# Kernel tuning notes

Measured on AMD Instinct MI355X. Metric: run time of the kernel, lower is better.

The kernel has to match this reference:

```python
import jax, jax.numpy as jnp
import numpy as np

B, C, H, W = 8, 128, 128, 128
C5 = 5 * C


def setup_inputs() -> dict:
    key = jax.random.key(0)
    ks = jax.random.split(key, 9)
    s_dw = 0.1   # depthwise weight scale
    s_pw = 0.02  # pointwise weight scale
    return {
        "x": jax.random.normal(ks[0], (B, C, H, W), jnp.float32),
        "w1": jax.random.normal(ks[1], (C5, 1, 1, 1), jnp.float32) * s_dw,
        "b1": jax.random.normal(ks[2], (C5,), jnp.float32) * 0.01,
        "w2": jax.random.normal(ks[3], (C5, 1, 3, 3), jnp.float32) * s_dw,
        "b2": jax.random.normal(ks[4], (C5,), jnp.float32) * 0.01,
        "w3": jax.random.normal(ks[5], (C5, 1, 3, 3), jnp.float32) * s_dw,
        "b3": jax.random.normal(ks[6], (C5,), jnp.float32) * 0.01,
        "w4": jax.random.normal(ks[7], (C, C5, 1, 1), jnp.float32) * s_pw,
        "b4": jax.random.normal(ks[8], (C,), jnp.float32) * 0.01,
    }


def nnstacking(x):
    # pad H,W by 1 then stack the 4-neighborhood + center along channels -> 5C
    p = jnp.pad(x, ((0, 0), (0, 0), (1, 1), (1, 1)))
    return jnp.concatenate(
        [p[:, :, 2:, 1:-1],   # neighbor below (i+1, j)
         p[:, :, :-2, 1:-1],  # neighbor above (i-1, j)
         p[:, :, 1:-1, 2:],   # neighbor right (i, j+1)
         p[:, :, 1:-1, :-2],  # neighbor left  (i, j-1)
         p[:, :, 1:-1, 1:-1]],  # center
        axis=1)


def _conv(x, w, b, dilation, padding, groups):
    y = jax.lax.conv_general_dilated(
        x, w, window_strides=(1, 1),
        padding=[(padding, padding), (padding, padding)],
        rhs_dilation=(dilation, dilation),
        dimension_numbers=("NCHW", "OIHW", "NCHW"),
        feature_group_count=groups)
    return y + b[None, :, None, None]


def reference(x, w1, b1, w2, b2, w3, b3, w4, b4):
    shortcut = x
    s = nnstacking(x)  # (B, 5C, H, W)
    # three depthwise branches (groups = 5C): 1x1 rate-1, 3x3 dil-8, 3x3 dil-12
    y = (_conv(s, w1, b1, 1, 0, C5)
         + _conv(s, w2, b2, 8, 8, C5)
         + _conv(s, w3, b3, 12, 12, C5))
    # pointwise 5C -> C, then residual add
    return _conv(y, w4, b4, 1, 0, 1) + shortcut
```

## Files before the change

### kernel.cpp

```cpp
#include <hip/hip_runtime.h>
#include <stdint.h>
#include <stddef.h>


static constexpr int Cc  = 128;
static constexpr int C5  = 640;
static constexpr int Hh  = 128;
static constexpr int Ww  = 128;
static constexpr int LC  = 160;
static constexpr int GR  = 42;
static constexpr int PSz = GR * LC + 8;

typedef __attribute__((ext_vector_type(8))) short short8;
typedef __attribute__((ext_vector_type(4))) float f32x4;

__device__ __forceinline__ uint16_t f2bf(float f) {
  uint32_t b = __float_as_uint(f);
  b += 0x7fffu + ((b >> 16) & 1u);
  return (uint16_t)(b >> 16);
}
__device__ __forceinline__ float bflo(uint32_t v) { return __uint_as_float(v << 16); }
__device__ __forceinline__ float bfhi(uint32_t v) { return __uint_as_float(v & 0xffff0000u); }

__device__ __forceinline__ void async16(uint16_t* lds, const uint16_t* gm) {
  __builtin_amdgcn_global_load_lds(
      (const __attribute__((address_space(1))) uint32_t*)gm,
      (__attribute__((address_space(3))) uint32_t*)lds, 16, 0, 0);
}

__global__ void prep_kernel(const float* __restrict__ w1, const float* __restrict__ b1,
                            const float* __restrict__ w2, const float* __restrict__ b2,
                            const float* __restrict__ w3, const float* __restrict__ b3,
                            const float* __restrict__ w4,
                            uint16_t* __restrict__ w4b, float* __restrict__ cw2,
                            float* __restrict__ cw3, float* __restrict__ bsum) {
  int i = blockIdx.x * 256 + threadIdx.x;
  if (i < Cc * C5) w4b[i] = f2bf(w4[i]);
  if (i < C5) {
    bsum[i] = b1[i] + b2[i] + b3[i];
#pragma unroll
    for (int t = 0; t < 9; ++t) {
      float a = w2[i * 9 + t];
      if (t == 4) a += w1[i] + w3[i * 9 + 4];
      cw2[i * 9 + t] = a;
      cw3[i * 9 + t] = w3[i * 9 + t];
    }
  }
}

__global__ __launch_bounds__(256, 2) void dw_kernel(
    const float* __restrict__ x, const float* __restrict__ cw2,
    const float* __restrict__ cw3, const float* __restrict__ bsum,
    uint16_t* __restrict__ y, int b0) {
  __shared__ uint16_t xs[4 * PSz];

  const int band = blockIdx.x;
  const int g    = blockIdx.y;
  const int bl   = blockIdx.z;
  const int bb   = b0 + bl;
  const int i0   = band * 16;
  const int tid  = threadIdx.x;

#pragma unroll
  for (int it = 0; it < 27; ++it) {
    int idx = it * 256 + tid;
    if (idx < 6720) {
      int col4 = idx % 40;
      int rr   = (idx / 40) % 42;
      int cel  = idx / 1680;
      int gi = i0 - 13 + rr;
      int gj = col4 * 4 - 16;
      float4 v = make_float4(0.f, 0.f, 0.f, 0.f);
      if ((unsigned)gi < 128u && col4 >= 4 && col4 < 36) {
        v = *(const float4*)(x + (((size_t)(bb * Cc + g * 4 + cel) * Hh + gi) << 7) + gj);
      }
      ushort4 h;
      h.x = f2bf(v.x); h.y = f2bf(v.y); h.z = f2bf(v.z); h.w = f2bf(v.w);
      *(ushort4*)(xs + cel * PSz + rr * LC + col4 * 4) = h;
    }
  }
  __syncthreads();

  const int ce = tid & 3;
  const int jt = (tid >> 2) & 7;
  const int ir = tid >> 5;
  const int j0 = jt * 16;
  const int c  = g * 4 + ce;

  float rb[48];
#define LOAD_RB(ROW)                                                      \
  do {                                                                    \
    const uint16_t* _p = xs + ce * PSz + (ROW) * LC + j0;                 \
    _Pragma("unroll") for (int _u = 0; _u < 6; ++_u) {                    \
      uint4 _q = *(const uint4*)(_p + _u * 8);                            \
      rb[_u * 8 + 0] = bflo(_q.x); rb[_u * 8 + 1] = bfhi(_q.x);           \
      rb[_u * 8 + 2] = bflo(_q.y); rb[_u * 8 + 3] = bfhi(_q.y);           \
      rb[_u * 8 + 4] = bflo(_q.z); rb[_u * 8 + 5] = bfhi(_q.z);           \
      rb[_u * 8 + 6] = bflo(_q.w); rb[_u * 8 + 7] = bfhi(_q.w);           \
    }                                                                     \
  } while (0)

  {
    float w2r[3][9], w3r[3][9], bs[3];
    const int msA[3] = {4, 2, 3};
#pragma unroll
    for (int mi = 0; mi < 3; ++mi) {
      int k = msA[mi] * Cc + c;
#pragma unroll
      for (int t = 0; t < 9; ++t) {
        w2r[mi][t] = cw2[k * 9 + t];
        w3r[mi][t] = cw3[k * 9 + t];
      }
      bs[mi] = bsum[k];
    }

#pragma unroll
    for (int it2 = 0; it2 < 2; ++it2) {
      const int i     = i0 + ir + 8 * it2;
      const int rbase = ir + 8 * it2 + 13;
      float acc[3][16];
#pragma unroll
      for (int mi = 0; mi < 3; ++mi)
#pragma unroll
        for (int jj = 0; jj < 16; ++jj) acc[mi][jj] = bs[mi];

#define AROW3(DLT, WARR, UB, DD)                                          \
      do {                                                                \
        LOAD_RB(rbase + (DLT));                                           \
        _Pragma("unroll") for (int mi = 0; mi < 3; ++mi) {                \
          const int aj = (mi == 0) ? 0 : ((mi == 1) ? 1 : -1);            \
          _Pragma("unroll") for (int v = 0; v < 3; ++v) {                 \
            const float w = WARR[mi][(UB) + v];                           \
            const int e = 16 + (DD) * (v - 1) + aj;                       \
            _Pragma("unroll") for (int jj = 0; jj < 16; ++jj)             \
              acc[mi][jj] += w * rb[e + jj];                              \
          }                                                               \
        }                                                                 \
      } while (0)

      AROW3(-12, w3r, 0, 12);
      if (j0 == 0)   acc[1][11] -= w3r[1][0] * rb[16];
      if (j0 == 112) acc[2][4]  -= w3r[2][2] * rb[31];

      AROW3(-8, w2r, 0, 8);
      if (j0 == 0)   acc[1][7]  -= w2r[1][0] * rb[16];
      if (j0 == 112) acc[2][8]  -= w2r[2][2] * rb[31];

      {
        LOAD_RB(rbase);
#pragma unroll
        for (int mi = 0; mi < 3; ++mi) {
          const int aj = (mi == 0) ? 0 : ((mi == 1) ? 1 : -1);
#pragma unroll
          for (int v = 0; v < 3; ++v) {
            const float w = w2r[mi][3 + v];
            const int e = 16 + 8 * (v - 1) + aj;
#pragma unroll
            for (int jj = 0; jj < 16; ++jj) acc[mi][jj] += w * rb[e + jj];
          }
          {
            const float w = w3r[mi][3]; const int e = 4 + aj;
#pragma unroll
            for (int jj = 0; jj < 16; ++jj) acc[mi][jj] += w * rb[e + jj];
          }
          {
            const float w = w3r[mi][5]; const int e = 28 + aj;
#pragma unroll
            for (int jj = 0; jj < 16; ++jj) acc[mi][jj] += w * rb[e + jj];
          }
        }
        if (j0 == 0)   { acc[1][7] -= w2r[1][3] * rb[16]; acc[1][11] -= w3r[1][3] * rb[16]; }
        if (j0 == 112) { acc[2][8] -= w2r[2][5] * rb[31]; acc[2][4]  -= w3r[2][5] * rb[31]; }
      }

      AROW3(8, w2r, 6, 8);
      if (j0 == 0)   acc[1][7]  -= w2r[1][6] * rb[16];
      if (j0 == 112) acc[2][8]  -= w2r[2][8] * rb[31];

      AROW3(12, w3r, 6, 12);
      if (j0 == 0)   acc[1][11] -= w3r[1][6] * rb[16];
      if (j0 == 112) acc[2][4]  -= w3r[2][8] * rb[31];
#undef AROW3

#pragma unroll
      for (int mi = 0; mi < 3; ++mi) {
        const int msA_[3] = {4, 2, 3};
        int k4 = msA_[mi] * 32 + g;
        size_t base = (((size_t)(bl * 160 + k4) << 14) + (size_t)i * Ww + j0) * 4 + ce;
#pragma unroll
        for (int jj = 0; jj < 16; ++jj) y[base + jj * 4] = f2bf(acc[mi][jj]);
      }
    }
  }

  {
    float w2r[2][9], w3r[2][9], bs[2];
#pragma unroll
    for (int mi = 0; mi < 2; ++mi) {
      int k = mi * Cc + c;
#pragma unroll
      for (int t = 0; t < 9; ++t) {
        w2r[mi][t] = cw2[k * 9 + t];
        w3r[mi][t] = cw3[k * 9 + t];
      }
      bs[mi] = bsum[k];
    }

#pragma unroll
    for (int it2 = 0; it2 < 2; ++it2) {
      const int i     = i0 + ir + 8 * it2;
      const int rbase = ir + 8 * it2 + 13;
      float acc[2][16];
#pragma unroll
      for (int mi = 0; mi < 2; ++mi)
#pragma unroll
        for (int jj = 0; jj < 16; ++jj) acc[mi][jj] = bs[mi];

#define BROW3(MI, DLT, WARR, UB, DD, BADROW)                              \
      do {                                                                \
        LOAD_RB(rbase + (DLT));                                           \
        const float sel = ((i + (DLT)) == (BADROW)) ? 0.f : 1.f;          \
        _Pragma("unroll") for (int v = 0; v < 3; ++v) {                   \
          const float w = WARR[MI][(UB) + v] * sel;                       \
          const int e = 16 + (DD) * (v - 1);                              \
          _Pragma("unroll") for (int jj = 0; jj < 16; ++jj)               \
            acc[MI][jj] += w * rb[e + jj];                                \
        }                                                                 \
      } while (0)

#define BROWC(MI, DLT, BADROW)                                            \
      do {                                                                \
        LOAD_RB(rbase + (DLT));                                           \
        const float sel = ((i + (DLT)) == (BADROW)) ? 0.f : 1.f;          \
        _Pragma("unroll") for (int v = 0; v < 3; ++v) {                   \
          const float w = w2r[MI][3 + v] * sel;                           \
          const int e = 16 + 8 * (v - 1);                                 \
          _Pragma("unroll") for (int jj = 0; jj < 16; ++jj)               \
            acc[MI][jj] += w * rb[e + jj];                                \
        }                                                                 \
        {                                                                 \
          const float w = w3r[MI][3] * sel;                               \
          _Pragma("unroll") for (int jj = 0; jj < 16; ++jj)               \
            acc[MI][jj] += w * rb[4 + jj];                                \
        }                                                                 \
        {                                                                 \
          const float w = w3r[MI][5] * sel;                               \
          _Pragma("unroll") for (int jj = 0; jj < 16; ++jj)               \
            acc[MI][jj] += w * rb[28 + jj];                               \
        }                                                                 \
      } while (0)

      BROW3(0, -11, w3r, 0, 12, 0);
      BROW3(0, -7,  w2r, 0, 8, 0);
      BROWC(0, 1, 0);
      BROW3(0, 9,   w2r, 6, 8, 0);
      BROW3(0, 13,  w3r, 6, 12, 0);
      BROW3(1, -13, w3r, 0, 12, 127);
      BROW3(1, -9,  w2r, 0, 8, 127);
      BROWC(1, -1, 127);
      BROW3(1, 7,   w2r, 6, 8, 127);
      BROW3(1, 11,  w3r, 6, 12, 127);
#undef BROW3
#undef BROWC

#pragma unroll
      for (int mi = 0; mi < 2; ++mi) {
        int k4 = mi * 32 + g;
        size_t base = (((size_t)(bl * 160 + k4) << 14) + (size_t)i * Ww + j0) * 4 + ce;
#pragma unroll
        for (int jj = 0; jj < 16; ++jj) y[base + jj * 4] = f2bf(acc[mi][jj]);
      }
    }
  }
#undef LOAD_RB
}

__global__ __launch_bounds__(256, 2) void gemm_kernel(
    const uint16_t* __restrict__ w4b, const uint16_t* __restrict__ y,
    const float* __restrict__ x, const float* __restrict__ b4,
    float* __restrict__ out, int b0) {
  __shared__ uint16_t As[128 * 64];
  __shared__ uint16_t Bs[16 * 128 * 4];

  const int tid  = threadIdx.x;
  const int lane = tid & 63;
  const int wave = tid >> 6;
  const int p0   = blockIdx.x * 128;
  const int bl   = blockIdx.y;
  const int bb   = b0 + bl;

  const int col = lane & 15;
  const int q   = lane >> 4;
  const int o_base = (wave >> 1) * 64;
  const int p_base = (wave & 1) * 64;

  f32x4 acc[4][4];
#pragma unroll
  for (int fm = 0; fm < 4; ++fm)
#pragma unroll
    for (int fn = 0; fn < 4; ++fn) acc[fm][fn] = (f32x4){0.f, 0.f, 0.f, 0.f};

  for (int kt = 0; kt < 10; ++kt) {
#pragma unroll
    for (int l = 0; l < 4; ++l) {
      int u  = (wave * 4 + l) * 64 + lane;
      int o  = u >> 3, ch = u & 7;
      async16(As + u * 8, w4b + (size_t)o * 640 + kt * 64 + ch * 8);
    }
#pragma unroll
    for (int l = 0; l < 4; ++l) {
      int k4t = wave * 4 + l;
      async16(Bs + (k4t * 64 + lane) * 8,
              y + (((size_t)(bl * 160 + kt * 16 + k4t) << 14) + p0) * 4 + lane * 8);
    }
    __syncthreads();

#pragma unroll
    for (int kk = 0; kk < 2; ++kk) {
      short8 af[4], bf[4];
#pragma unroll
      for (int fm = 0; fm < 4; ++fm) {
        int o = o_base + fm * 16 + col;
        af[fm] = *(const short8*)(As + o * 64 + kk * 32 + q * 8);
      }
#pragma unroll
      for (int fn = 0; fn < 4; ++fn) {
        int p = p_base + fn * 16 + col;
        union { short8 s; uint32_t u[4]; } bu;
        const uint32_t* lo = (const uint32_t*)(Bs + ((kk * 8 + 2 * q) * 128 + p) * 4);
        const uint32_t* hi = (const uint32_t*)(Bs + ((kk * 8 + 2 * q + 1) * 128 + p) * 4);
        bu.u[0] = lo[0]; bu.u[1] = lo[1]; bu.u[2] = hi[0]; bu.u[3] = hi[1];
        bf[fn] = bu.s;
      }
#pragma unroll
      for (int fm = 0; fm < 4; ++fm)
#pragma unroll
        for (int fn = 0; fn < 4; ++fn)
          acc[fm][fn] = __builtin_amdgcn_mfma_f32_16x16x32_bf16(af[fm], bf[fn], acc[fm][fn], 0, 0, 0);
    }
    __syncthreads();
  }

#pragma unroll
  for (int fm = 0; fm < 4; ++fm) {
#pragma unroll
    for (int fn = 0; fn < 4; ++fn) {
      int pg = p0 + p_base + fn * 16 + col;
#pragma unroll
      for (int r = 0; r < 4; ++r) {
        int oo = o_base + fm * 16 + q * 4 + r;
        size_t oi = ((size_t)(bb * 128 + oo) << 14) + pg;
        out[oi] = acc[fm][fn][r] + b4[oo] + x[oi];
      }
    }
  }
}

extern "C" void kernel_launch(void* const* d_in, const int* in_sizes, int n_in,
                              void* d_out, int out_size, void* d_ws, size_t ws_size,
                              hipStream_t stream) {
  const float* x  = (const float*)d_in[0];
  const float* w1 = (const float*)d_in[1];
  const float* b1 = (const float*)d_in[2];
  const float* w2 = (const float*)d_in[3];
  const float* b2 = (const float*)d_in[4];
  const float* w3 = (const float*)d_in[5];
  const float* b3 = (const float*)d_in[6];
  const float* w4 = (const float*)d_in[7];
  const float* b4 = (const float*)d_in[8];
  float* out = (float*)d_out;

  char* ws = (char*)d_ws;
  uint16_t* w4b  = (uint16_t*)ws;
  float*    cw2  = (float*)(ws + 163840);
  float*    cw3  = (float*)(ws + 186880);
  float*    bsum = (float*)(ws + 209920);
  uint16_t* y    = (uint16_t*)(ws + (1 << 20));

  const size_t per_b = (size_t)160 * 16384 * 4 * 2;
  int nbc = 4;
  while (nbc > 1 && (size_t)(1 << 20) + (size_t)nbc * per_b > ws_size) nbc >>= 1;

  hipLaunchKernelGGL(prep_kernel, dim3(320), dim3(256), 0, stream,
                     w1, b1, w2, b2, w3, b3, w4, w4b, cw2, cw3, bsum);
  for (int b0 = 0; b0 < 8; b0 += nbc) {
    int nb = (8 - b0) < nbc ? (8 - b0) : nbc;
    hipLaunchKernelGGL(dw_kernel, dim3(8, 32, nb), dim3(256), 0, stream,
                       x, cw2, cw3, bsum, y, b0);
    hipLaunchKernelGGL(gemm_kernel, dim3(128, nb), dim3(256), 0, stream,
                       w4b, y, x, b4, out, b0);
  }
}
```

Baseline: 334.1 us.

## Load GEMM operands directly from global into registers with double buffering

The pointwise GEMM kernel no longer stages A and B tiles in LDS. Each wave now loads its MFMA fragments straight from global memory into registers, with a two-stage register double buffer that prefetches the next K tile while the current one is multiplied, and all __syncthreads are gone. Launch bounds drop to one block per CU to make room for the extra registers. The batch chunk size is raised to 8 so the depthwise and GEMM kernels each run over all batches in one launch when the workspace allows it. The risks are uncoalesced, redundant global reads (each wave re-reads operands other waves also need), lower occupancy, and a larger workspace footprint.

```diff
diff --git a/kernel.cpp b/kernel.cpp
--- a/kernel.cpp
+++ b/kernel.cpp
@@ -21,12 +21,6 @@
 }
 __device__ __forceinline__ float bflo(uint32_t v) { return __uint_as_float(v << 16); }
 __device__ __forceinline__ float bfhi(uint32_t v) { return __uint_as_float(v & 0xffff0000u); }
-
-__device__ __forceinline__ void async16(uint16_t* lds, const uint16_t* gm) {
-  __builtin_amdgcn_global_load_lds(
-      (const __attribute__((address_space(1))) uint32_t*)gm,
-      (__attribute__((address_space(3))) uint32_t*)lds, 16, 0, 0);
-}
 
 __global__ void prep_kernel(const float* __restrict__ w1, const float* __restrict__ b1,
                             const float* __restrict__ w2, const float* __restrict__ b2,
@@ -275,13 +269,10 @@
 #undef LOAD_RB
 }
 
-__global__ __launch_bounds__(256, 2) void gemm_kernel(
+__global__ __launch_bounds__(256, 1) void gemm_kernel(
     const uint16_t* __restrict__ w4b, const uint16_t* __restrict__ y,
     const float* __restrict__ x, const float* __restrict__ b4,
     float* __restrict__ out, int b0) {
-  __shared__ uint16_t As[128 * 64];
-  __shared__ uint16_t Bs[16 * 128 * 4];
-
   const int tid  = threadIdx.x;
   const int lane = tid & 63;
   const int wave = tid >> 6;
@@ -300,46 +291,60 @@
 #pragma unroll
     for (int fn = 0; fn < 4; ++fn) acc[fm][fn] = (f32x4){0.f, 0.f, 0.f, 0.f};
 
-  for (int kt = 0; kt < 10; ++kt) {
-#pragma unroll
-    for (int l = 0; l < 4; ++l) {
-      int u  = (wave * 4 + l) * 64 + lane;
-      int o  = u >> 3, ch = u & 7;
-      async16(As + u * 8, w4b + (size_t)o * 640 + kt * 64 + ch * 8);
-    }
-#pragma unroll
-    for (int l = 0; l < 4; ++l) {
-      int k4t = wave * 4 + l;
-      async16(Bs + (k4t * 64 + lane) * 8,
-              y + (((size_t)(bl * 160 + kt * 16 + k4t) << 14) + p0) * 4 + lane * 8);
-    }
-    __syncthreads();
-
-#pragma unroll
-    for (int kk = 0; kk < 2; ++kk) {
-      short8 af[4], bf[4];
-#pragma unroll
-      for (int fm = 0; fm < 4; ++fm) {
-        int o = o_base + fm * 16 + col;
-        af[fm] = *(const short8*)(As + o * 64 + kk * 32 + q * 8);
-      }
-#pragma unroll
-      for (int fn = 0; fn < 4; ++fn) {
-        int p = p_base + fn * 16 + col;
-        union { short8 s; uint32_t u[4]; } bu;
-        const uint32_t* lo = (const uint32_t*)(Bs + ((kk * 8 + 2 * q) * 128 + p) * 4);
-        const uint32_t* hi = (const uint32_t*)(Bs + ((kk * 8 + 2 * q + 1) * 128 + p) * 4);
-        bu.u[0] = lo[0]; bu.u[1] = lo[1]; bu.u[2] = hi[0]; bu.u[3] = hi[1];
-        bf[fn] = bu.s;
-      }
-#pragma unroll
-      for (int fm = 0; fm < 4; ++fm)
-#pragma unroll
-        for (int fn = 0; fn < 4; ++fn)
-          acc[fm][fn] = __builtin_amdgcn_mfma_f32_16x16x32_bf16(af[fm], bf[fn], acc[fm][fn], 0, 0, 0);
-    }
-    __syncthreads();
-  }
+#define LOADA(AF, KT, KK)                                                   \
+  do {                                                                      \
+    _Pragma("unroll") for (int fm = 0; fm < 4; ++fm) {                      \
+      int o = o_base + fm * 16 + col;                                       \
+      AF[fm] = *(const short8*)(w4b + (size_t)o * 640 + (KT) * 64 +         \
+                                (KK) * 32 + q * 8);                         \
+    }                                                                       \
+  } while (0)
+
+#define LOADB(BF, KT, KK)                                                   \
+  do {                                                                      \
+    _Pragma("unroll") for (int fn = 0; fn < 4; ++fn) {                      \
+      int p = p0 + p_base + fn * 16 + col;                                  \
+      size_t rlo = (((size_t)(bl * 160 + (KT) * 16 + (KK) * 8 + 2 * q)      \
+                     << 14) + p) * 4;                                       \
+      union { short8 s; uint32_t u[4]; } bu;                                \
+      const uint32_t* lo = (const uint32_t*)(y + rlo);                      \
+      const uint32_t* hi = (const uint32_t*)(y + rlo + ((size_t)1 << 16));  \
+      bu.u[0] = lo[0]; bu.u[1] = lo[1]; bu.u[2] = hi[0]; bu.u[3] = hi[1];   \
+      BF[fn] = bu.s;                                                        \
+    }                                                                       \
+  } while (0)
+
+#define MFMAS(AF0, BF0, AF1, BF1)                                           \
+  do {                                                                      \
+    _Pragma("unroll") for (int fm = 0; fm < 4; ++fm)                        \
+      _Pragma("unroll") for (int fn = 0; fn < 4; ++fn)                      \
+        acc[fm][fn] = __builtin_amdgcn_mfma_f32_16x16x32_bf16(              \
+            AF0[fm], BF0[fn], acc[fm][fn], 0, 0, 0);                        \
+    _Pragma("unroll") for (int fm = 0; fm < 4; ++fm)                        \
+      _Pragma("unroll") for (int fn = 0; fn < 4; ++fn)                      \
+        acc[fm][fn] = __builtin_amdgcn_mfma_f32_16x16x32_bf16(              \
+            AF1[fm], BF1[fn], acc[fm][fn], 0, 0, 0);                        \
+  } while (0)
+
+  short8 aA[2][4], bA[2][4];
+  short8 aB[2][4], bB[2][4];
+  LOADA(aA[0], 0, 0); LOADA(aA[1], 0, 1);
+  LOADB(bA[0], 0, 0); LOADB(bA[1], 0, 1);
+
+#pragma unroll
+  for (int kt = 0; kt < 10; kt += 2) {
+    LOADA(aB[0], kt + 1, 0); LOADA(aB[1], kt + 1, 1);
+    LOADB(bB[0], kt + 1, 0); LOADB(bB[1], kt + 1, 1);
+    MFMAS(aA[0], bA[0], aA[1], bA[1]);
+    if (kt + 2 < 10) {
+      LOADA(aA[0], kt + 2, 0); LOADA(aA[1], kt + 2, 1);
+      LOADB(bA[0], kt + 2, 0); LOADB(bA[1], kt + 2, 1);
+    }
+    MFMAS(aB[0], bB[0], aB[1], bB[1]);
+  }
+#undef LOADA
+#undef LOADB
+#undef MFMAS
 
 #pragma unroll
   for (int fm = 0; fm < 4; ++fm) {
@@ -378,7 +383,7 @@
   uint16_t* y    = (uint16_t*)(ws + (1 << 20));
 
   const size_t per_b = (size_t)160 * 16384 * 4 * 2;
-  int nbc = 4;
+  int nbc = 8;
   while (nbc > 1 && (size_t)(1 << 20) + (size_t)nbc * per_b > ws_size) nbc >>= 1;
 
   hipLaunchKernelGGL(prep_kernel, dim3(320), dim3(256), 0, stream,
```

New measurement: 359.4 us. +7.6%, slower.

## Double-buffer GEMM shared-memory tiles and process all batches per launch

Applied to the files above, without the earlier changes.

Splits the GEMM kernel's LDS A/B tiles into two buffers so the async global-to-LDS copy for the next K-tile is issued before computing on the current one, overlapping load latency with MFMA work. LDS use per block doubles (to about 64KB), which may limit the two-blocks-per-CU occupancy the launch bounds ask for. Separately, the batch chunk size rises from 4 to 8 so, when the workspace is large enough, the depthwise and GEMM kernels are each launched once over all batches. This needs a larger intermediate buffer and gives less cache locality between the two stages.

```diff
diff --git a/kernel.cpp b/kernel.cpp
--- a/kernel.cpp
+++ b/kernel.cpp
@@ -279,8 +279,8 @@
     const uint16_t* __restrict__ w4b, const uint16_t* __restrict__ y,
     const float* __restrict__ x, const float* __restrict__ b4,
     float* __restrict__ out, int b0) {
-  __shared__ uint16_t As[128 * 64];
-  __shared__ uint16_t Bs[16 * 128 * 4];
+  __shared__ uint16_t As[2][128 * 64];
+  __shared__ uint16_t Bs[2][16 * 128 * 4];
 
   const int tid  = threadIdx.x;
   const int lane = tid & 63;
@@ -300,46 +300,60 @@
 #pragma unroll
     for (int fn = 0; fn < 4; ++fn) acc[fm][fn] = (f32x4){0.f, 0.f, 0.f, 0.f};
 
-  for (int kt = 0; kt < 10; ++kt) {
-#pragma unroll
-    for (int l = 0; l < 4; ++l) {
-      int u  = (wave * 4 + l) * 64 + lane;
-      int o  = u >> 3, ch = u & 7;
-      async16(As + u * 8, w4b + (size_t)o * 640 + kt * 64 + ch * 8);
-    }
-#pragma unroll
-    for (int l = 0; l < 4; ++l) {
-      int k4t = wave * 4 + l;
-      async16(Bs + (k4t * 64 + lane) * 8,
-              y + (((size_t)(bl * 160 + kt * 16 + k4t) << 14) + p0) * 4 + lane * 8);
-    }
+#define STAGE(BUF, KT)                                                      \
+  do {                                                                      \
+    _Pragma("unroll") for (int l = 0; l < 4; ++l) {                         \
+      int u  = (wave * 4 + l) * 64 + lane;                                  \
+      int o  = u >> 3, ch = u & 7;                                          \
+      async16(As[BUF] + u * 8, w4b + (size_t)o * 640 + (KT) * 64 + ch * 8); \
+    }                                                                       \
+    _Pragma("unroll") for (int l = 0; l < 4; ++l) {                         \
+      int k4t = wave * 4 + l;                                               \
+      async16(Bs[BUF] + (k4t * 64 + lane) * 8,                              \
+              y + (((size_t)(bl * 160 + (KT) * 16 + k4t) << 14) + p0) * 4   \
+                + lane * 8);                                                \
+    }                                                                       \
+  } while (0)
+
+#define COMPUTE(BUF)                                                        \
+  do {                                                                      \
+    _Pragma("unroll") for (int kk = 0; kk < 2; ++kk) {                      \
+      short8 af[4], bf[4];                                                  \
+      _Pragma("unroll") for (int fm = 0; fm < 4; ++fm) {                    \
+        int o = o_base + fm * 16 + col;                                     \
+        af[fm] = *(const short8*)(As[BUF] + o * 64 + kk * 32 + q * 8);      \
+      }                                                                     \
+      _Pragma("unroll") for (int fn = 0; fn < 4; ++fn) {                    \
+        int p = p_base + fn * 16 + col;                                     \
+        union { short8 s; uint32_t u[4]; } bu;                              \
+        const uint32_t* lo =                                                \
+            (const uint32_t*)(Bs[BUF] + ((kk * 8 + 2 * q) * 128 + p) * 4);  \
+        const uint32_t* hi =                                                \
+            (const uint32_t*)(Bs[BUF] + ((kk * 8 + 2 * q + 1) * 128 + p) * 4); \
+        bu.u[0] = lo[0]; bu.u[1] = lo[1]; bu.u[2] = hi[0]; bu.u[3] = hi[1]; \
+        bf[fn] = bu.s;                                                      \
+      }                                                                     \
+      _Pragma("unroll") for (int fm = 0; fm < 4; ++fm)                      \
+        _Pragma("unroll") for (int fn = 0; fn < 4; ++fn)                    \
+          acc[fm][fn] = __builtin_amdgcn_mfma_f32_16x16x32_bf16(            \
+              af[fm], bf[fn], acc[fm][fn], 0, 0, 0);                        \
+    }                                                                       \
+  } while (0)
+
+  STAGE(0, 0);
+  __syncthreads();
+
+#pragma unroll
+  for (int kt = 0; kt < 10; kt += 2) {
+    STAGE(1, kt + 1);
+    COMPUTE(0);
     __syncthreads();
-
-#pragma unroll
-    for (int kk = 0; kk < 2; ++kk) {
-      short8 af[4], bf[4];
-#pragma unroll
-      for (int fm = 0; fm < 4; ++fm) {
-        int o = o_base + fm * 16 + col;
-        af[fm] = *(const short8*)(As + o * 64 + kk * 32 + q * 8);
-      }
-#pragma unroll
-      for (int fn = 0; fn < 4; ++fn) {
-        int p = p_base + fn * 16 + col;
-        union { short8 s; uint32_t u[4]; } bu;
-        const uint32_t* lo = (const uint32_t*)(Bs + ((kk * 8 + 2 * q) * 128 + p) * 4);
-        const uint32_t* hi = (const uint32_t*)(Bs + ((kk * 8 + 2 * q + 1) * 128 + p) * 4);
-        bu.u[0] = lo[0]; bu.u[1] = lo[1]; bu.u[2] = hi[0]; bu.u[3] = hi[1];
-        bf[fn] = bu.s;
-      }
-#pragma unroll
-      for (int fm = 0; fm < 4; ++fm)
-#pragma unroll
-        for (int fn = 0; fn < 4; ++fn)
-          acc[fm][fn] = __builtin_amdgcn_mfma_f32_16x16x32_bf16(af[fm], bf[fn], acc[fm][fn], 0, 0, 0);
-    }
+    if (kt + 2 < 10) STAGE(0, kt + 2);
+    COMPUTE(1);
     __syncthreads();
   }
+#undef STAGE
+#undef COMPUTE
 
 #pragma unroll
   for (int fm = 0; fm < 4; ++fm) {
@@ -378,7 +392,7 @@
   uint16_t* y    = (uint16_t*)(ws + (1 << 20));
 
   const size_t per_b = (size_t)160 * 16384 * 4 * 2;
-  int nbc = 4;
+  int nbc = 8;
   while (nbc > 1 && (size_t)(1 << 20) + (size_t)nbc * per_b > ws_size) nbc >>= 1;
 
   hipLaunchKernelGGL(prep_kernel, dim3(320), dim3(256), 0, stream,
```

After: 336.3 us. About the same (+0.7%).
